# Performance work log

Measured on AMD Instinct MI355X. Metric: run time of the kernel, lower is better.

## Reference

```python
import jax, jax.numpy as jnp
import numpy as np

B, S, D = 2, 4096, 1024
H, DK = 16, 64          # heads, QK feature dim per head
DV = D // H             # output features per head = 64
QKV_OUT = (2 * DK + DV) * H  # 3072


def setup_inputs() -> dict:
    key = jax.random.key(0)
    k1, k2, k3, k4, k5 = jax.random.split(key, 5)
    x = jax.random.normal(k1, (B, S, D), dtype=jnp.float32)
    Wqkv = jax.random.normal(k2, (D, QKV_OUT), dtype=jnp.float32) * (1.0 / np.sqrt(D))
    bqkv = jnp.zeros((QKV_OUT,), dtype=jnp.float32)
    Wproj = jax.random.normal(k3, (D, D), dtype=jnp.float32) * (1.0 / np.sqrt(D))
    bproj = jnp.zeros((D,), dtype=jnp.float32)
    return {"x": x, "Wqkv": Wqkv, "bqkv": bqkv, "Wproj": Wproj, "bproj": bproj}


def reference(x, Wqkv, bqkv, Wproj, bproj):
    # QKV projection: [B,S,(2*DK+DV)*H]
    qkv = x @ Wqkv + bqkv
    q_len = DK * H
    Q = qkv[:, :, :q_len].reshape(B, S, H, DK).transpose(0, 2, 1, 3)        # [B,H,S,DK]
    K = qkv[:, :, q_len:2 * q_len].reshape(B, S, H, DK).transpose(0, 2, 1, 3)
    V = qkv[:, :, 2 * q_len:].reshape(B, S, H, DV).transpose(0, 2, 1, 3)    # [B,H,S,DV]

    scores = jnp.einsum("bhqd,bhkd->bhqk", Q, K) * (1.0 / np.sqrt(DK))
    # Faithful to source: causal mask is tril(ones) with zeros -> -inf,
    # i.e. +1.0 is ADDED on allowed positions (harmless constant shift per row).
    tril = jnp.tril(jnp.ones((S, S), dtype=jnp.float32))
    mask = jnp.where(tril == 0, -jnp.inf, tril)
    scores = scores + mask
    attn = jax.nn.softmax(scores, axis=-1)  # dropout disabled (p=0 / eval)

    out = jnp.einsum("bhqk,bhkd->bhqd", attn, V)            # [B,H,S,DV]
    out = out.transpose(0, 2, 1, 3).reshape(B, S, H * DV)   # [B,S,D]
    return out @ Wproj + bproj
```

## Files before the change

kernel.cpp:

```cpp
#include <hip/hip_runtime.h>
#include <stdint.h>


typedef __bf16 bf16x8 __attribute__((ext_vector_type(8)));
typedef float f32x4 __attribute__((ext_vector_type(4)));
typedef unsigned short u16x8 __attribute__((ext_vector_type(8)));
typedef unsigned short u16x4 __attribute__((ext_vector_type(4)));
typedef unsigned int u32x4 __attribute__((ext_vector_type(4)));

__device__ __forceinline__ unsigned short f2bf(float f) {
  unsigned u = __builtin_bit_cast(unsigned, f);
  u += 0x7FFFu + ((u >> 16) & 1u);
  return (unsigned short)(u >> 16);
}

__device__ __forceinline__ float fast_exp2(float x) {
#if __has_builtin(__builtin_amdgcn_exp2f)
  return __builtin_amdgcn_exp2f(x);
#else
  return exp2f(x);
#endif
}

__device__ __forceinline__ void gload16(const void* g, void* l) {
  __builtin_amdgcn_global_load_lds(
      (__attribute__((address_space(1))) unsigned int*)(uintptr_t)g,
      (__attribute__((address_space(3))) unsigned int*)(unsigned int)(uintptr_t)l,
      16, 0, 0);
}

__global__ void k_cvt_bf16(const float* __restrict__ in,
                           unsigned short* __restrict__ out, int n8) {
  int i = blockIdx.x * blockDim.x + threadIdx.x;
  if (i >= n8) return;
  const float4* p = reinterpret_cast<const float4*>(in) + (size_t)i * 2;
  float4 a = p[0], b = p[1];
  u16x8 o;
  o[0] = f2bf(a.x); o[1] = f2bf(a.y); o[2] = f2bf(a.z); o[3] = f2bf(a.w);
  o[4] = f2bf(b.x); o[5] = f2bf(b.y); o[6] = f2bf(b.z); o[7] = f2bf(b.w);
  *(reinterpret_cast<u16x8*>(out) + i) = o;
}

__global__ void k_transcvt(const float* __restrict__ in,
                           unsigned short* __restrict__ out, int K, int N) {
  __shared__ float tile[32][33];
  int tk0 = blockIdx.y << 5, tn0 = blockIdx.x << 5;
  int t = threadIdx.x;
  int r = t >> 3, c4 = (t & 7) << 2;
  float4 v = *reinterpret_cast<const float4*>(&in[(size_t)(tk0 + r) * N + tn0 + c4]);
  tile[r][c4 + 0] = v.x; tile[r][c4 + 1] = v.y;
  tile[r][c4 + 2] = v.z; tile[r][c4 + 3] = v.w;
  __syncthreads();
  u16x4 o;
  o[0] = f2bf(tile[c4 + 0][r]); o[1] = f2bf(tile[c4 + 1][r]);
  o[2] = f2bf(tile[c4 + 2][r]); o[3] = f2bf(tile[c4 + 3][r]);
  *reinterpret_cast<u16x4*>(&out[(size_t)(tn0 + r) * K + tk0 + c4]) = o;
}

__device__ __forceinline__ void gemm_core_db(
    const unsigned short* __restrict__ A, const unsigned short* __restrict__ Bt,
    unsigned short (*Al)[128 * 32], unsigned short (*Bl)[128 * 32],
    int m0, int n0, f32x4 acc[4][4]) {
  const int t = threadIdx.x;
  const int lane = t & 63;
  const int w = t >> 6;
  const int wr = w >> 1, wc = w & 1;
  const int l15 = lane & 15, l4 = lane >> 4;

  const int c0 = t, c1 = t + 256;
  const int r0 = c0 >> 2, s0 = ((c0 & 3) << 3) ^ (((r0 >> 1) & 3) << 3);
  const int r1 = c1 >> 2, s1 = ((c1 & 3) << 3) ^ (((r1 >> 1) & 3) << 3);
  const size_t ga0 = (size_t)(m0 + r0) * 1024 + s0;
  const size_t ga1 = (size_t)(m0 + r1) * 1024 + s1;
  const size_t gb0 = (size_t)(n0 + r0) * 1024 + s0;
  const size_t gb1 = (size_t)(n0 + r1) * 1024 + s1;

  int aidx[4], bidx[4];
#pragma unroll
  for (int m = 0; m < 4; ++m) {
    int row = wr * 64 + m * 16 + l15;
    aidx[m] = row * 32 + ((l4 * 8) ^ (((row >> 1) & 3) << 3));
    row = wc * 64 + m * 16 + l15;
    bidx[m] = row * 32 + ((l4 * 8) ^ (((row >> 1) & 3) << 3));
  }

#define GSTAGE(bufi, kofs)                                   \
  do {                                                       \
    gload16(A + ga0 + (kofs), Al[bufi] + c0 * 8);            \
    gload16(A + ga1 + (kofs), Al[bufi] + c1 * 8);            \
    gload16(Bt + gb0 + (kofs), Bl[bufi] + c0 * 8);           \
    gload16(Bt + gb1 + (kofs), Bl[bufi] + c1 * 8);           \
  } while (0)

  GSTAGE(0, 0);
  asm volatile("s_waitcnt vmcnt(0)" ::: "memory");
  __builtin_amdgcn_s_barrier();

#pragma unroll 1
  for (int it = 0; it < 32; ++it) {
    const int cur = it & 1;
    if (it + 1 < 32) GSTAGE(cur ^ 1, (it + 1) * 32);
    bf16x8 af[4], bfr[4];
#pragma unroll
    for (int m = 0; m < 4; ++m)
      af[m] = *reinterpret_cast<const bf16x8*>(Al[cur] + aidx[m]);
#pragma unroll
    for (int n = 0; n < 4; ++n)
      bfr[n] = *reinterpret_cast<const bf16x8*>(Bl[cur] + bidx[n]);
    __builtin_amdgcn_s_setprio(1);
#pragma unroll
    for (int m = 0; m < 4; ++m)
#pragma unroll
      for (int n = 0; n < 4; ++n)
        acc[m][n] = __builtin_amdgcn_mfma_f32_16x16x32_bf16(af[m], bfr[n],
                                                            acc[m][n], 0, 0, 0);
    __builtin_amdgcn_s_setprio(0);
    asm volatile("s_waitcnt vmcnt(0)" ::: "memory");
    __builtin_amdgcn_s_barrier();
  }
#undef GSTAGE
}

__global__ __launch_bounds__(256) void k_gemm_qkv(
    const unsigned short* __restrict__ A, const unsigned short* __restrict__ Bt,
    const float* __restrict__ bias, unsigned short* __restrict__ Qb,
    unsigned short* __restrict__ Kb, unsigned short* __restrict__ VTb) {
  __shared__ unsigned short Al[2][128 * 32];
  __shared__ unsigned short Bl[2][128 * 32];
  const int lane = threadIdx.x & 63, w = threadIdx.x >> 6;
  const int wr = w >> 1, wc = w & 1;
  const int l15 = lane & 15, l4 = lane >> 4;
  const int m0 = blockIdx.y << 7, n0 = blockIdx.x << 7;
  const float C1 = 0.18033688011112043f;

  f32x4 acc[4][4] = {};
  gemm_core_db(A, Bt, Al, Bl, m0, n0, acc);

  float bi[4];
#pragma unroll
  for (int n = 0; n < 4; ++n) bi[n] = bias[n0 + wc * 64 + n * 16 + l15];

  if (n0 < 2048) {
#pragma unroll
    for (int m = 0; m < 4; ++m)
#pragma unroll
      for (int n = 0; n < 4; ++n)
#pragma unroll
        for (int j = 0; j < 4; ++j) {
          int row = m0 + wr * 64 + m * 16 + l4 * 4 + j;
          int col = n0 + wc * 64 + n * 16 + l15;
          float v = acc[m][n][j] + bi[n];
          int b = row >> 12, s = row & 4095;
          if (col < 1024) {
            int hh = col >> 6, d = col & 63;
            Qb[((size_t)(b * 16 + hh) * 4096 + s) * 64 + d] = f2bf(v * C1);
          } else {
            int cc = col - 1024; int hh = cc >> 6, d = cc & 63;
            Kb[((size_t)(b * 16 + hh) * 4096 + s) * 64 + d] = f2bf(v);
          }
        }
  } else {
#pragma unroll
    for (int m = 0; m < 4; ++m)
#pragma unroll
      for (int n = 0; n < 4; ++n) {
        int row0 = m0 + wr * 64 + m * 16 + l4 * 4;
        int cc = n0 - 2048 + wc * 64 + n * 16 + l15;
        int b = row0 >> 12, s0 = row0 & 4095;
        int hh = cc >> 6, d = cc & 63;
        u16x4 pk;
#pragma unroll
        for (int j = 0; j < 4; ++j) pk[j] = f2bf(acc[m][n][j] + bi[n]);
        *reinterpret_cast<u16x4*>(
            &VTb[((size_t)(b * 16 + hh) * 64 + d) * 4096 + s0]) = pk;
      }
  }
}

__global__ __launch_bounds__(256) void k_gemm_proj(
    const unsigned short* __restrict__ A, const unsigned short* __restrict__ Bt,
    const float* __restrict__ bias, float* __restrict__ out) {
  __shared__ unsigned short Al[2][128 * 32];
  __shared__ unsigned short Bl[2][128 * 32];
  const int lane = threadIdx.x & 63, w = threadIdx.x >> 6;
  const int wr = w >> 1, wc = w & 1;
  const int l15 = lane & 15, l4 = lane >> 4;
  const int m0 = blockIdx.y << 7, n0 = blockIdx.x << 7;

  f32x4 acc[4][4] = {};
  gemm_core_db(A, Bt, Al, Bl, m0, n0, acc);

#pragma unroll
  for (int m = 0; m < 4; ++m) {
#pragma unroll
    for (int n = 0; n < 4; ++n) {
#pragma unroll
      for (int j = 0; j < 4; ++j) {
        int row = m0 + wr * 64 + m * 16 + l4 * 4 + j;
        int col = n0 + wc * 64 + n * 16 + l15;
        out[(size_t)row * 1024 + col] = acc[m][n][j] + bias[col];
      }
    }
  }
}

__global__ __launch_bounds__(256, 4) void k_attn(
    const unsigned short* __restrict__ Qb, const unsigned short* __restrict__ Kb,
    const unsigned short* __restrict__ VTb, unsigned short* __restrict__ Ob) {
  __shared__ unsigned short Kl[2][64 * 64];
  __shared__ unsigned short Vl[2][64 * 64];
  const int t = threadIdx.x;
  const int lane = t & 63, w = t >> 6;
  const int l15 = lane & 15, l4 = lane >> 4;
  const int idx = blockIdx.x;
  const int r = idx >> 8;
  const int g = (idx >> 5) & 7;
  const int bh = idx & 31;
  const int qt = (r == 0) ? (31 - g) : (r == 1) ? (16 + g)
               : (r == 2) ? (15 - g) : g;
  const size_t qkbase = (size_t)bh * 4096 * 64;
  const size_t vbase = (size_t)bh * 64 * 4096;
  const int b = bh >> 4, hh = bh & 15;
  const int wrow0 = qt * 128 + w * 32;
  const int nt = 2 * qt + 2;

  const int c0 = t, c1 = t + 256;
  const int kr0 = c0 >> 3, ks0 = ((c0 & 7) << 3) ^ ((kr0 & 7) << 3);
  const int kr1 = c1 >> 3, ks1 = ((c1 & 7) << 3) ^ ((kr1 & 7) << 3);

#define STAGE(bufi, jt)                                                             \
  do {                                                                              \
    gload16(Kb + qkbase + (size_t)((jt) * 64 + kr0) * 64 + ks0, &Kl[bufi][c0 * 8]); \
    gload16(Kb + qkbase + (size_t)((jt) * 64 + kr1) * 64 + ks1, &Kl[bufi][c1 * 8]); \
    gload16(VTb + vbase + (size_t)kr0 * 4096 + (jt) * 64 + ks0, &Vl[bufi][c0 * 8]); \
    gload16(VTb + vbase + (size_t)kr1 * 4096 + (jt) * 64 + ks1, &Vl[bufi][c1 * 8]); \
  } while (0)

  bf16x8 qf[2][2];
#pragma unroll
  for (int m = 0; m < 2; ++m)
#pragma unroll
    for (int kk = 0; kk < 2; ++kk)
      qf[m][kk] = *reinterpret_cast<const bf16x8*>(
          &Qb[qkbase + (size_t)(wrow0 + m * 16 + l15) * 64 + kk * 32 + l4 * 8]);

  u16x8 ones_u;
#pragma unroll
  for (int i = 0; i < 8; ++i) ones_u[i] = 0x3F80;
  const bf16x8 onesf = __builtin_bit_cast(bf16x8, ones_u);

  f32x4 oacc[2][4] = {};
  f32x4 lacc[2] = {};

  STAGE(0, 0);
  asm volatile("s_waitcnt vmcnt(0)" ::: "memory");
  __builtin_amdgcn_s_barrier();

  for (int j = 0; j < nt; ++j) {
    const int cur = j & 1;
    if (j + 1 < nt) STAGE(cur ^ 1, j + 1);

    const int jk0 = j * 64;
    const bool active = (jk0 <= wrow0 + 31);
    const bool needmask = active && (jk0 + 63 > wrow0);

    if (active) {
#pragma unroll
      for (int h = 0; h < 2; ++h) {
        f32x4 sch[2][2] = {};
        __builtin_amdgcn_s_setprio(1);
#pragma unroll
        for (int nn = 0; nn < 2; ++nn) {
          int krow = (h * 2 + nn) * 16 + l15;
#pragma unroll
          for (int kk = 0; kk < 2; ++kk) {
            int kcol = (kk * 32 + l4 * 8) ^ ((krow & 7) << 3);
            bf16x8 kfr = *reinterpret_cast<const bf16x8*>(&Kl[cur][krow * 64 + kcol]);
#pragma unroll
            for (int m = 0; m < 2; ++m)
              sch[m][nn] = __builtin_amdgcn_mfma_f32_16x16x32_bf16(
                  kfr, qf[m][kk], sch[m][nn], 0, 0, 0);
          }
        }
        __builtin_amdgcn_s_setprio(0);

        bf16x8 pa[2];
#pragma unroll
        for (int m = 0; m < 2; ++m) {
#pragma unroll
          for (int nn = 0; nn < 2; ++nn)
#pragma unroll
            for (int r2 = 0; r2 < 4; ++r2)
              sch[m][nn][r2] = fast_exp2(sch[m][nn][r2]);
          if (needmask) {
            const int qg = wrow0 + m * 16 + l15;
#pragma unroll
            for (int nn = 0; nn < 2; ++nn) {
              const int kb = jk0 + (h * 2 + nn) * 16 + l4 * 4;
#pragma unroll
              for (int r2 = 0; r2 < 4; ++r2)
                if (kb + r2 > qg) sch[m][nn][r2] = 0.f;
            }
          }
          unsigned A0, A1, B0, B1;
          asm("v_cvt_pk_bf16_f32 %0, %1, %2"
              : "=v"(A0) : "v"(sch[m][0][0]), "v"(sch[m][0][1]));
          asm("v_cvt_pk_bf16_f32 %0, %1, %2"
              : "=v"(A1) : "v"(sch[m][0][2]), "v"(sch[m][0][3]));
          asm("v_cvt_pk_bf16_f32 %0, %1, %2"
              : "=v"(B0) : "v"(sch[m][1][0]), "v"(sch[m][1][1]));
          asm("v_cvt_pk_bf16_f32 %0, %1, %2"
              : "=v"(B1) : "v"(sch[m][1][2]), "v"(sch[m][1][3]));
          asm("v_permlane32_swap_b32 %0, %1" : "+v"(A0), "+v"(B0));
          asm("v_permlane16_swap_b32 %0, %1" : "+v"(A0), "+v"(B0));
          asm("v_permlane32_swap_b32 %0, %1" : "+v"(A1), "+v"(B1));
          asm("v_permlane16_swap_b32 %0, %1" : "+v"(A1), "+v"(B1));
          u32x4 pw;
          pw[0] = A0; pw[1] = A1; pw[2] = B0; pw[3] = B1;
          pa[m] = __builtin_bit_cast(bf16x8, pw);
        }

        __builtin_amdgcn_s_setprio(1);
        lacc[0] = __builtin_amdgcn_mfma_f32_16x16x32_bf16(pa[0], onesf, lacc[0], 0, 0, 0);
        lacc[1] = __builtin_amdgcn_mfma_f32_16x16x32_bf16(pa[1], onesf, lacc[1], 0, 0, 0);
#pragma unroll
        for (int nn2 = 0; nn2 < 4; ++nn2) {
          int vr = nn2 * 16 + l15;
          int vc = (h * 32 + l4 * 8) ^ ((vr & 7) << 3);
          bf16x8 vf = *reinterpret_cast<const bf16x8*>(&Vl[cur][vr * 64 + vc]);
          oacc[0][nn2] = __builtin_amdgcn_mfma_f32_16x16x32_bf16(
              pa[0], vf, oacc[0][nn2], 0, 0, 0);
          oacc[1][nn2] = __builtin_amdgcn_mfma_f32_16x16x32_bf16(
              pa[1], vf, oacc[1][nn2], 0, 0, 0);
        }
        __builtin_amdgcn_s_setprio(0);
      }
    }

    asm volatile("s_waitcnt vmcnt(0)" ::: "memory");
    __builtin_amdgcn_s_barrier();
  }
#undef STAGE

#pragma unroll
  for (int m = 0; m < 2; ++m)
#pragma unroll
    for (int jj = 0; jj < 4; ++jj) {
      float inv = 1.0f / lacc[m][jj];
      int srow = wrow0 + m * 16 + l4 * 4 + jj;
#pragma unroll
      for (int nn = 0; nn < 4; ++nn) {
        int col = hh * 64 + nn * 16 + l15;
        Ob[((size_t)(b * 4096 + srow)) * 1024 + col] =
            __builtin_bit_cast(unsigned short, (__bf16)(oacc[m][nn][jj] * inv));
      }
    }
}

extern "C" void kernel_launch(void* const* d_in, const int* in_sizes, int n_in,
                              void* d_out, int out_size, void* d_ws, size_t ws_size,
                              hipStream_t stream) {
  const float* x = (const float*)d_in[0];
  const float* Wqkv = (const float*)d_in[1];
  const float* bqkv = (const float*)d_in[2];
  const float* Wproj = (const float*)d_in[3];
  const float* bproj = (const float*)d_in[4];

  char* ws = (char*)d_ws;
  unsigned short* xb  = (unsigned short*)(ws);
  unsigned short* Wqb = (unsigned short*)(ws + 16777216);
  unsigned short* Wpb = (unsigned short*)(ws + 23068672);
  unsigned short* Qb  = (unsigned short*)(ws + 25165824);
  unsigned short* Kb  = (unsigned short*)(ws + 41943040);
  unsigned short* VTb = (unsigned short*)(ws + 58720256);
  unsigned short* Ob  = (unsigned short*)(ws + 75497472);

  k_cvt_bf16<<<dim3(8388608 / 8 / 256), dim3(256), 0, stream>>>(x, xb, 8388608 / 8);
  k_transcvt<<<dim3(3072 / 32, 1024 / 32), dim3(256), 0, stream>>>(Wqkv, Wqb, 1024, 3072);
  k_transcvt<<<dim3(1024 / 32, 1024 / 32), dim3(256), 0, stream>>>(Wproj, Wpb, 1024, 1024);
  k_gemm_qkv<<<dim3(3072 / 128, 8192 / 128), dim3(256), 0, stream>>>(xb, Wqb, bqkv, Qb, Kb, VTb);
  k_attn<<<dim3(1024), dim3(256), 0, stream>>>(Qb, Kb, VTb, Ob);
  k_gemm_proj<<<dim3(1024 / 128, 8192 / 128), dim3(256), 0, stream>>>(Ob, Wpb, bproj, (float*)d_out);
}
```

Baseline: 200.6 us.

## Switch GEMM K-loop from double to triple-buffered LDS ring with prefetch distance two

Converts the shared GEMM core used by the QKV and output projection kernels from a two-slot to a three-slot LDS ring buffer. Loads are issued two iterations ahead, and the wait uses vmcnt(4) so only the older stage must be complete before the barrier. The goal is to hide more global-to-LDS latency behind MFMA work. In exchange, LDS use per block rises from 32KB to 48KB, which can lower occupancy, and the waitcnt bookkeeping becomes more delicate.

Measured after the change: 198.8 us. About the same (-0.9%).

```diff
diff --git a/kernel.cpp b/kernel.cpp
--- a/kernel.cpp
+++ b/kernel.cpp
@@ -57,7 +57,7 @@
   *reinterpret_cast<u16x4*>(&out[(size_t)(tn0 + r) * K + tk0 + c4]) = o;
 }
 
-__device__ __forceinline__ void gemm_core_db(
+__device__ __forceinline__ void gemm_core_r3(
     const unsigned short* __restrict__ A, const unsigned short* __restrict__ Bt,
     unsigned short (*Al)[128 * 32], unsigned short (*Bl)[128 * 32],
     int m0, int n0, f32x4 acc[4][4]) {
@@ -84,22 +84,25 @@
     bidx[m] = row * 32 + ((l4 * 8) ^ (((row >> 1) & 3) << 3));
   }
 
-#define GSTAGE(bufi, kofs)                                   \
+#define GSTAGE(sl, kofs)                                     \
   do {                                                       \
-    gload16(A + ga0 + (kofs), Al[bufi] + c0 * 8);            \
-    gload16(A + ga1 + (kofs), Al[bufi] + c1 * 8);            \
-    gload16(Bt + gb0 + (kofs), Bl[bufi] + c0 * 8);           \
-    gload16(Bt + gb1 + (kofs), Bl[bufi] + c1 * 8);           \
+    gload16(A + ga0 + (kofs), Al[sl] + c0 * 8);              \
+    gload16(A + ga1 + (kofs), Al[sl] + c1 * 8);              \
+    gload16(Bt + gb0 + (kofs), Bl[sl] + c0 * 8);             \
+    gload16(Bt + gb1 + (kofs), Bl[sl] + c1 * 8);             \
   } while (0)
 
   GSTAGE(0, 0);
-  asm volatile("s_waitcnt vmcnt(0)" ::: "memory");
+  GSTAGE(1, 32);
+  asm volatile("s_waitcnt vmcnt(4)" ::: "memory");
   __builtin_amdgcn_s_barrier();
 
+  int cur = 0;
 #pragma unroll 1
   for (int it = 0; it < 32; ++it) {
-    const int cur = it & 1;
-    if (it + 1 < 32) GSTAGE(cur ^ 1, (it + 1) * 32);
+    int nxt = cur + 1; if (nxt == 3) nxt = 0;
+    int pre = nxt + 1; if (pre == 3) pre = 0;
+    if (it + 2 < 32) GSTAGE(pre, (it + 2) * 32);
     bf16x8 af[4], bfr[4];
 #pragma unroll
     for (int m = 0; m < 4; ++m)
@@ -115,8 +118,13 @@
         acc[m][n] = __builtin_amdgcn_mfma_f32_16x16x32_bf16(af[m], bfr[n],
                                                             acc[m][n], 0, 0, 0);
     __builtin_amdgcn_s_setprio(0);
-    asm volatile("s_waitcnt vmcnt(0)" ::: "memory");
-    __builtin_amdgcn_s_barrier();
+    if (it + 2 < 32) {
+      asm volatile("s_waitcnt vmcnt(4)" ::: "memory");
+    } else if (it + 1 < 32) {
+      asm volatile("s_waitcnt vmcnt(0)" ::: "memory");
+    }
+    if (it + 1 < 32) __builtin_amdgcn_s_barrier();
+    cur = nxt;
   }
 #undef GSTAGE
 }
@@ -125,8 +133,8 @@
     const unsigned short* __restrict__ A, const unsigned short* __restrict__ Bt,
     const float* __restrict__ bias, unsigned short* __restrict__ Qb,
     unsigned short* __restrict__ Kb, unsigned short* __restrict__ VTb) {
-  __shared__ unsigned short Al[2][128 * 32];
-  __shared__ unsigned short Bl[2][128 * 32];
+  __shared__ unsigned short Al[3][128 * 32];
+  __shared__ unsigned short Bl[3][128 * 32];
   const int lane = threadIdx.x & 63, w = threadIdx.x >> 6;
   const int wr = w >> 1, wc = w & 1;
   const int l15 = lane & 15, l4 = lane >> 4;
@@ -134,7 +142,7 @@
   const float C1 = 0.18033688011112043f;
 
   f32x4 acc[4][4] = {};
-  gemm_core_db(A, Bt, Al, Bl, m0, n0, acc);
+  gemm_core_r3(A, Bt, Al, Bl, m0, n0, acc);
 
   float bi[4];
 #pragma unroll
@@ -180,15 +188,15 @@
 __global__ __launch_bounds__(256) void k_gemm_proj(
     const unsigned short* __restrict__ A, const unsigned short* __restrict__ Bt,
     const float* __restrict__ bias, float* __restrict__ out) {
-  __shared__ unsigned short Al[2][128 * 32];
-  __shared__ unsigned short Bl[2][128 * 32];
+  __shared__ unsigned short Al[3][128 * 32];
+  __shared__ unsigned short Bl[3][128 * 32];
   const int lane = threadIdx.x & 63, w = threadIdx.x >> 6;
   const int wr = w >> 1, wc = w & 1;
   const int l15 = lane & 15, l4 = lane >> 4;
   const int m0 = blockIdx.y << 7, n0 = blockIdx.x << 7;
 
   f32x4 acc[4][4] = {};
-  gemm_core_db(A, Bt, Al, Bl, m0, n0, acc);
+  gemm_core_r3(A, Bt, Al, Bl, m0, n0, acc);
 
 #pragma unroll
   for (int m = 0; m < 4; ++m) {
```
